# Kernel tuning notes

Measured on AMD Instinct MI355X. Metric: run time of the kernel, lower is better.

The kernel has to match this reference:

```python
import jax, jax.numpy as jnp
import numpy as np

# Module hyperparameters (from init_kwargs / config defaults)
LOCAL_WINDOW = 128
GLOBAL_BUDGET = 64
ATT_BUDGET = 0.05
RANDOM_BUDGET = 0.1

B, S, D = 4, 4096, 1024


def setup_inputs() -> dict:
    key = jax.random.key(0)
    k1, k2 = jax.random.split(key)
    return {
        "hidden_states": jax.random.normal(k1, (B, S, D), dtype=jnp.float32),
        "attention_mask": jnp.ones((B, S), dtype=jnp.int32),
        "W_imp": jax.random.normal(k2, (1, D), dtype=jnp.float32) * 0.02,
    }


def _build_sparse_mask(hidden_states, attention_mask, W_imp):
    b, s, d = hidden_states.shape
    valid = attention_mask.astype(bool)                       # [b, s]
    # base mask: valid x valid, with causal constraint (is_decoder=True)
    i = jnp.arange(s)[:, None]
    j = jnp.arange(s)[None, :]
    causal = j <= i                                            # [s, s]
    base = (valid[:, None, :] & valid[:, :, None]) & causal[None]

    # 1) local causal sliding window: query i attends keys in [i-W+1, i]
    diff = i - j
    local = (diff >= 0) & (diff < LOCAL_WINDOW)                # [s, s]
    sparse = jnp.broadcast_to(local[None], (b, s, s))
    selected = jnp.broadcast_to(local.any(axis=0)[None], (b, s))

    # 2) global tokens via importance projection + top-k
    base_budget = min(GLOBAL_BUDGET, max(1, int(s * ATT_BUDGET)))
    scores = jnp.einsum('bsd,d->bs', hidden_states, W_imp[0])  # [b, s]
    scores = jnp.where(valid, scores, -jnp.inf)
    _, top_idx = jax.lax.top_k(scores, base_budget)            # [b, k]
    global_tokens = jnp.zeros((b, s), bool).at[
        jnp.arange(b)[:, None], top_idx].set(True)             # [b, s]
    # globals attend to everything and are attended by everything
    sparse = sparse | global_tokens[:, None, :] | global_tokens[:, :, None]
    selected = selected | global_tokens

    # 3) structured random tokens: deterministic strided selection
    r_budget = min(s, max(1, int(s * RANDOM_BUDGET)))
    stride = max(1, s // r_budget)
    rand_idx = (jnp.arange(r_budget) * stride) % s
    random_1d = jnp.zeros((s,), bool).at[rand_idx].set(True)
    random_tokens = jnp.broadcast_to(random_1d[None], (b, s))  # [b, s]
    sparse = sparse | random_tokens[:, None, :] | random_tokens[:, :, None]
    selected = selected | random_tokens

    # re-apply validity + causality
    sparse = sparse & base
    return sparse, selected, global_tokens, random_tokens


def reference(hidden_states, attention_mask, W_imp):
    b, s, _ = hidden_states.shape
    sparse, selected, gtok, rtok = _build_sparse_mask(
        hidden_states, attention_mask, W_imp)
    total_connections = sparse.sum(axis=(1, 2))
    attention_efficiency = total_connections.astype(jnp.float32) / float(s * s)
    # return sparse mask as float (the form consumed by attention), plus stats
    return (sparse.astype(jnp.float32), selected, attention_efficiency)
```

## Files before the change

kernel.cpp:

```cpp
#include <hip/hip_runtime.h>
#include <math.h>

#define BATCH 4
#define SEQ   4096
#define DIM   1024
#define TOPK  64
#define RSTRIDE 10
#define RBUDGET 409
#define LOCALW  128

typedef float nfloat4 __attribute__((ext_vector_type(4)));

#define WS_SCORES_OFF 0
#define WS_FLAGS_OFF  (BATCH * SEQ * sizeof(float))

__global__ void scores_kernel(const float* __restrict__ hs,
                              const int* __restrict__ amask,
                              const float* __restrict__ W,
                              float* __restrict__ scores) {
    int row  = blockIdx.x * 4 + (threadIdx.x >> 6);
    int lane = threadIdx.x & 63;
    const float4* h4 = (const float4*)(hs + (size_t)row * DIM);
    const float4* w4 = (const float4*)W;
    float acc = 0.0f;
#pragma unroll
    for (int k = 0; k < DIM / 4 / 64; ++k) {
        float4 h = h4[lane + 64 * k];
        float4 w = w4[lane + 64 * k];
        acc += h.x * w.x + h.y * w.y + h.z * w.z + h.w * w.w;
    }
#pragma unroll
    for (int off = 32; off; off >>= 1) acc += __shfl_down(acc, off, 64);
    if (lane == 0)
        scores[row] = amask[row] ? acc : -INFINITY;
}

__global__ void topk_fused_kernel(const float* __restrict__ scores,
                                  const int* __restrict__ amask,
                                  unsigned char* __restrict__ flags,
                                  float* __restrict__ out_selected,
                                  float* __restrict__ out_eff) {
    __shared__ unsigned int su[SEQ];
    __shared__ int cumH[SEQ];
    __shared__ unsigned char gsel[SEQ];
    __shared__ unsigned char sflags[SEQ];
    __shared__ unsigned int hist[257];
    __shared__ unsigned int sufA[257];
    __shared__ unsigned int sufB[257];
    __shared__ unsigned int bcast[2];
    __shared__ int tvA[256], tvB[256], thA[256], thB[256], red[256];

    int b = blockIdx.x, t = threadIdx.x;

    for (int k = t; k < SEQ; k += 256) {
        float s = scores[b * SEQ + k];
        unsigned int x = __float_as_uint(s);
        su[k] = (x & 0x80000000u) ? ~x : (x | 0x80000000u);
        gsel[k] = 0;
    }
    __syncthreads();

    unsigned int prefixVal = 0;
    unsigned int remaining = TOPK;
#pragma unroll
    for (int pass = 0; pass < 4; ++pass) {
        int shift = 24 - 8 * pass;
        unsigned int highmask = (pass == 0) ? 0u : (0xFFFFFFFFu << (shift + 8));

        hist[t] = 0;
        if (t == 0) hist[256] = 0;
        __syncthreads();
#pragma unroll
        for (int e = 0; e < SEQ / 256; ++e) {
            unsigned int u = su[t * (SEQ / 256) + e];
            if ((u & highmask) == prefixVal)
                atomicAdd(&hist[(u >> shift) & 0xFFu], 1u);
        }
        __syncthreads();

        sufA[t] = hist[t];
        if (t == 0) sufA[256] = 0;
        __syncthreads();
        unsigned int* src = sufA;
        unsigned int* dst = sufB;
        for (int d = 1; d < 256; d <<= 1) {
            unsigned int v = src[t] + ((t + d < 256) ? src[t + d] : 0u);
            dst[t] = v;
            if (t == 0) dst[256] = 0;
            __syncthreads();
            unsigned int* tmp = src; src = dst; dst = tmp;
        }
        if (src[t] >= remaining && src[t + 1] < remaining) {
            bcast[0] = (unsigned int)t;
            bcast[1] = remaining - src[t + 1];
        }
        __syncthreads();
        prefixVal |= (bcast[0] << shift);
        remaining = bcast[1];
        __syncthreads();
    }

    unsigned int T = prefixVal;
    unsigned int myeq = 0;
#pragma unroll
    for (int e = 0; e < SEQ / 256; ++e)
        if (su[t * (SEQ / 256) + e] == T) myeq++;
    sufA[t] = myeq;
    __syncthreads();
    {
        unsigned int* src = sufA;
        unsigned int* dst = sufB;
        for (int d = 1; d < 256; d <<= 1) {
            unsigned int v = src[t] + ((t >= d) ? src[t - d] : 0u);
            dst[t] = v;
            __syncthreads();
            unsigned int* tmp = src; src = dst; dst = tmp;
        }
        unsigned int taken = src[t] - myeq;
#pragma unroll
        for (int e = 0; e < SEQ / 256; ++e) {
            int idx = t * (SEQ / 256) + e;
            unsigned int u = su[idx];
            if (u > T) gsel[idx] = 1;
            else if (u == T) { if (taken < remaining) gsel[idx] = 1; taken++; }
        }
    }
    __syncthreads();

    for (int k = t; k < SEQ; k += 256) {
        int valid = (amask[b * SEQ + k] != 0) ? 1 : 0;
        int g = gsel[k];
        int r = ((k % RSTRIDE) == 0 && (k / RSTRIDE) < RBUDGET) ? 1 : 0;
        unsigned char f = (unsigned char)(valid | (g << 1) | (r << 2));
        flags[b * SEQ + k] = f;
        sflags[k] = f;
        out_selected[b * SEQ + k] = 1.0f;
    }
    __syncthreads();

    int* cumV = (int*)su;
    int lv[16], lh[16];
    int sv = 0, sh = 0;
#pragma unroll
    for (int e = 0; e < 16; ++e) {
        unsigned char f = sflags[t * 16 + e];
        int v = f & 1;
        int h = v & (((f & 6) != 0) ? 1 : 0);
        sv += v; sh += h;
        lv[e] = sv; lh[e] = sh;
    }
    tvA[t] = sv; thA[t] = sh;
    __syncthreads();
    int* vsrc = tvA; int* vdst = tvB;
    int* hsrc = thA; int* hdst = thB;
    for (int d = 1; d < 256; d <<= 1) {
        int av = vsrc[t] + ((t >= d) ? vsrc[t - d] : 0);
        int ah = hsrc[t] + ((t >= d) ? hsrc[t - d] : 0);
        vdst[t] = av; hdst[t] = ah;
        __syncthreads();
        int* tmp = vsrc; vsrc = vdst; vdst = tmp;
        tmp = hsrc; hsrc = hdst; hdst = tmp;
    }
    int bv = vsrc[t] - sv, bh = hsrc[t] - sh;
#pragma unroll
    for (int e = 0; e < 16; ++e) {
        cumV[t * 16 + e] = lv[e] + bv;
        cumH[t * 16 + e] = lh[e] + bh;
    }
    __syncthreads();

    int cnt = 0;
#pragma unroll
    for (int e = 0; e < 16; ++e) {
        int i = t * 16 + e;
        unsigned char f = sflags[i];
        int validI = f & 1;
        int hotI = (f & 6) != 0;
        int c;
        if (hotI) c = cumV[i];
        else {
            int w = (i >= LOCALW) ? (cumV[i] - cumV[i - LOCALW]) : cumV[i];
            int g = (i >= LOCALW) ? cumH[i - LOCALW] : 0;
            c = w + g;
        }
        cnt += validI ? c : 0;
    }
    red[t] = cnt;
    __syncthreads();
    for (int s2 = 128; s2; s2 >>= 1) {
        if (t < s2) red[t] += red[t + s2];
        __syncthreads();
    }
    if (t == 0)
        out_eff[b] = (float)red[0] * (1.0f / ((float)SEQ * (float)SEQ));
}

#define MASK_BLOCKS 8192
__global__ void __launch_bounds__(256) mask_kernel(
        const unsigned char* __restrict__ flags,
        float* __restrict__ out) {
    const uchar4* f4all = (const uchar4*)flags;
    nfloat4* out4 = (nfloat4*)out;
    int p = blockIdx.x * 256 + threadIdx.x;
    const int stride = MASK_BLOCKS * 256;
#pragma unroll
    for (int it = 0; it < (BATCH * SEQ * SEQ / 4) / (MASK_BLOCKS * 256); ++it) {
        int row = p >> 10;
        int i = row & (SEQ - 1);
        int bbase = (row >> 12) << 10;
        unsigned char fi = flags[row];
        int validI = fi & 1;
        int hotI = (fi & 6) != 0;
        int jg = p & 1023;
        uchar4 fj = f4all[bbase + jg];
        unsigned char fja[4] = {fj.x, fj.y, fj.z, fj.w};
        int j0 = jg << 2;
        nfloat4 v;
#pragma unroll
        for (int e = 0; e < 4; ++e) {
            int j = j0 + e;
            unsigned char f = fja[e];
            int one = (j <= i) & validI & (int)(f & 1)
                    & (((i - j) < LOCALW) | hotI | (int)((f & 6) != 0));
            v[e] = one ? 1.0f : 0.0f;
        }
        out4[p] = v;
        p += stride;
    }
}

extern "C" void kernel_launch(void* const* d_in, const int* in_sizes, int n_in,
                              void* d_out, int out_size, void* d_ws, size_t ws_size,
                              hipStream_t stream) {
    const float* hs    = (const float*)d_in[0];
    const int*   amask = (const int*)d_in[1];
    const float* W     = (const float*)d_in[2];

    char* ws = (char*)d_ws;
    float*         scores = (float*)(ws + WS_SCORES_OFF);
    unsigned char* flags  = (unsigned char*)(ws + WS_FLAGS_OFF);

    float* out_sparse   = (float*)d_out;
    float* out_selected = out_sparse + (size_t)BATCH * SEQ * SEQ;
    float* out_eff      = out_selected + BATCH * SEQ;

    scores_kernel<<<BATCH * SEQ / 4, 256, 0, stream>>>(hs, amask, W, scores);
    topk_fused_kernel<<<BATCH, 256, 0, stream>>>(scores, amask, flags,
                                                 out_selected, out_eff);
    mask_kernel<<<MASK_BLOCKS, 256, 0, stream>>>(flags, out_sparse);
}
```

Before: 337.7 us.

## Fuse scores, top-k and mask into one persistent kernel with grid barriers

Merges the three kernels into a single persistent kernel of 1008 blocks that uses software grid barriers. While four blocks run the top-k and efficiency computation, the remaining blocks write the zero upper-triangle half of the mask, so that store traffic overlaps the serial top-k phase. After the barrier only the lower triangle is computed from the flags. This relies on every block being co-resident for the spin barrier and adds a small init kernel to reset the barrier counters.

```diff
diff --git a/kernel.cpp b/kernel.cpp
--- a/kernel.cpp
+++ b/kernel.cpp
@@ -9,223 +9,265 @@
 #define RBUDGET 409
 #define LOCALW  128
 
+#define NBLK  1008
+#define NTOPK 4
+
 typedef float nfloat4 __attribute__((ext_vector_type(4)));
 
 #define WS_SCORES_OFF 0
 #define WS_FLAGS_OFF  (BATCH * SEQ * sizeof(float))
-
-__global__ void scores_kernel(const float* __restrict__ hs,
-                              const int* __restrict__ amask,
-                              const float* __restrict__ W,
-                              float* __restrict__ scores) {
-    int row  = blockIdx.x * 4 + (threadIdx.x >> 6);
-    int lane = threadIdx.x & 63;
-    const float4* h4 = (const float4*)(hs + (size_t)row * DIM);
-    const float4* w4 = (const float4*)W;
-    float acc = 0.0f;
-#pragma unroll
-    for (int k = 0; k < DIM / 4 / 64; ++k) {
-        float4 h = h4[lane + 64 * k];
-        float4 w = w4[lane + 64 * k];
-        acc += h.x * w.x + h.y * w.y + h.z * w.z + h.w * w.w;
-    }
-#pragma unroll
-    for (int off = 32; off; off >>= 1) acc += __shfl_down(acc, off, 64);
-    if (lane == 0)
-        scores[row] = amask[row] ? acc : -INFINITY;
-}
-
-__global__ void topk_fused_kernel(const float* __restrict__ scores,
-                                  const int* __restrict__ amask,
-                                  unsigned char* __restrict__ flags,
-                                  float* __restrict__ out_selected,
-                                  float* __restrict__ out_eff) {
+#define WS_SYNC_OFF   (WS_FLAGS_OFF + BATCH * SEQ)
+
+__global__ void init_sync_kernel(unsigned int* sync) {
+    if (threadIdx.x < 4) sync[threadIdx.x] = 0u;
+}
+
+__device__ __forceinline__ void grid_barrier(unsigned int* cnt,
+                                             unsigned int* flag) {
+    __syncthreads();
+    if (threadIdx.x == 0) {
+        __threadfence();
+        unsigned int old = atomicAdd(cnt, 1u);
+        if (old == (unsigned int)NBLK - 1u) {
+            __hip_atomic_store(flag, 1u, __ATOMIC_RELEASE,
+                               __HIP_MEMORY_SCOPE_AGENT);
+        } else {
+            while (__hip_atomic_load(flag, __ATOMIC_ACQUIRE,
+                                     __HIP_MEMORY_SCOPE_AGENT) == 0u) {}
+        }
+        __threadfence();
+    }
+    __syncthreads();
+}
+
+__global__ void __launch_bounds__(256, 4) fused_kernel(
+        const float* __restrict__ hs,
+        const int* __restrict__ amask,
+        const float* __restrict__ W,
+        float* scores,
+        unsigned char* flags,
+        unsigned int* sync,
+        float* out_sparse,
+        float* __restrict__ out_selected,
+        float* __restrict__ out_eff) {
     __shared__ unsigned int su[SEQ];
-    __shared__ int cumH[SEQ];
-    __shared__ unsigned char gsel[SEQ];
+    __shared__ unsigned short cumH[SEQ];
     __shared__ unsigned char sflags[SEQ];
     __shared__ unsigned int hist[257];
     __shared__ unsigned int sufA[257];
     __shared__ unsigned int sufB[257];
     __shared__ unsigned int bcast[2];
-    __shared__ int tvA[256], tvB[256], thA[256], thB[256], red[256];
-
-    int b = blockIdx.x, t = threadIdx.x;
-
-    for (int k = t; k < SEQ; k += 256) {
-        float s = scores[b * SEQ + k];
-        unsigned int x = __float_as_uint(s);
-        su[k] = (x & 0x80000000u) ? ~x : (x | 0x80000000u);
-        gsel[k] = 0;
-    }
-    __syncthreads();
-
-    unsigned int prefixVal = 0;
-    unsigned int remaining = TOPK;
-#pragma unroll
-    for (int pass = 0; pass < 4; ++pass) {
-        int shift = 24 - 8 * pass;
-        unsigned int highmask = (pass == 0) ? 0u : (0xFFFFFFFFu << (shift + 8));
-
-        hist[t] = 0;
-        if (t == 0) hist[256] = 0;
-        __syncthreads();
-#pragma unroll
-        for (int e = 0; e < SEQ / 256; ++e) {
-            unsigned int u = su[t * (SEQ / 256) + e];
-            if ((u & highmask) == prefixVal)
-                atomicAdd(&hist[(u >> shift) & 0xFFu], 1u);
-        }
-        __syncthreads();
-
-        sufA[t] = hist[t];
-        if (t == 0) sufA[256] = 0;
-        __syncthreads();
-        unsigned int* src = sufA;
-        unsigned int* dst = sufB;
+    __shared__ int tvA[256], tvB[256], thA[256], thB[256];
+    __shared__ int red[256];
+
+    const int bid = blockIdx.x;
+    const int t = threadIdx.x;
+
+    {
+        int lane = t & 63;
+        int wid = t >> 6;
+        const float4* w4 = (const float4*)W;
+        for (int row = bid * 4 + wid; row < BATCH * SEQ; row += NBLK * 4) {
+            const float4* h4 = (const float4*)(hs + (size_t)row * DIM);
+            float acc = 0.0f;
+#pragma unroll
+            for (int k = 0; k < DIM / 4 / 64; ++k) {
+                float4 h = h4[lane + 64 * k];
+                float4 w = w4[lane + 64 * k];
+                acc += h.x * w.x + h.y * w.y + h.z * w.z + h.w * w.w;
+            }
+#pragma unroll
+            for (int off = 32; off; off >>= 1) acc += __shfl_down(acc, off, 64);
+            if (lane == 0)
+                scores[row] = amask[row] ? acc : -INFINITY;
+        }
+        int gid = bid * 256 + t;
+        if (gid < BATCH * SEQ) out_selected[gid] = 1.0f;
+    }
+    grid_barrier(&sync[0], &sync[1]);
+
+    if (bid < NTOPK) {
+        int b = bid;
+        for (int k = t; k < SEQ; k += 256) {
+            float s = scores[b * SEQ + k];
+            unsigned int x = __float_as_uint(s);
+            su[k] = (x & 0x80000000u) ? ~x : (x | 0x80000000u);
+            sflags[k] = 0;
+        }
+        __syncthreads();
+
+        unsigned int prefixVal = 0;
+        unsigned int remaining = TOPK;
+#pragma unroll
+        for (int pass = 0; pass < 4; ++pass) {
+            int shift = 24 - 8 * pass;
+            unsigned int highmask = (pass == 0) ? 0u : (0xFFFFFFFFu << (shift + 8));
+
+            hist[t] = 0;
+            if (t == 0) hist[256] = 0;
+            __syncthreads();
+#pragma unroll
+            for (int e = 0; e < SEQ / 256; ++e) {
+                unsigned int u = su[t * (SEQ / 256) + e];
+                if ((u & highmask) == prefixVal)
+                    atomicAdd(&hist[(u >> shift) & 0xFFu], 1u);
+            }
+            __syncthreads();
+
+            sufA[t] = hist[t];
+            if (t == 0) sufA[256] = 0;
+            __syncthreads();
+            unsigned int* src = sufA;
+            unsigned int* dst = sufB;
+            for (int d = 1; d < 256; d <<= 1) {
+                unsigned int v = src[t] + ((t + d < 256) ? src[t + d] : 0u);
+                dst[t] = v;
+                if (t == 0) dst[256] = 0;
+                __syncthreads();
+                unsigned int* tmp = src; src = dst; dst = tmp;
+            }
+            if (src[t] >= remaining && src[t + 1] < remaining) {
+                bcast[0] = (unsigned int)t;
+                bcast[1] = remaining - src[t + 1];
+            }
+            __syncthreads();
+            prefixVal |= (bcast[0] << shift);
+            remaining = bcast[1];
+            __syncthreads();
+        }
+
+        unsigned int T = prefixVal;
+        unsigned int myeq = 0;
+#pragma unroll
+        for (int e = 0; e < SEQ / 256; ++e)
+            if (su[t * (SEQ / 256) + e] == T) myeq++;
+        sufA[t] = myeq;
+        __syncthreads();
+        {
+            unsigned int* src = sufA;
+            unsigned int* dst = sufB;
+            for (int d = 1; d < 256; d <<= 1) {
+                unsigned int v = src[t] + ((t >= d) ? src[t - d] : 0u);
+                dst[t] = v;
+                __syncthreads();
+                unsigned int* tmp = src; src = dst; dst = tmp;
+            }
+            unsigned int taken = src[t] - myeq;
+#pragma unroll
+            for (int e = 0; e < SEQ / 256; ++e) {
+                int idx = t * (SEQ / 256) + e;
+                unsigned int u = su[idx];
+                if (u > T) sflags[idx] |= 2;
+                else if (u == T) { if (taken < remaining) sflags[idx] |= 2; taken++; }
+            }
+        }
+        __syncthreads();
+
+        for (int k = t; k < SEQ; k += 256) {
+            int valid = (amask[b * SEQ + k] != 0) ? 1 : 0;
+            int g = (sflags[k] >> 1) & 1;
+            int r = ((k % RSTRIDE) == 0 && (k / RSTRIDE) < RBUDGET) ? 1 : 0;
+            unsigned char f = (unsigned char)(valid | (g << 1) | (r << 2));
+            sflags[k] = f;
+            flags[b * SEQ + k] = f;
+        }
+        __syncthreads();
+
+        int* cumV = (int*)su;
+        int lv[16], lh[16];
+        int sv = 0, sh = 0;
+#pragma unroll
+        for (int e = 0; e < 16; ++e) {
+            unsigned char f = sflags[t * 16 + e];
+            int v = f & 1;
+            int h = v & (((f & 6) != 0) ? 1 : 0);
+            sv += v; sh += h;
+            lv[e] = sv; lh[e] = sh;
+        }
+        tvA[t] = sv; thA[t] = sh;
+        __syncthreads();
+        int* vsrc = tvA; int* vdst = tvB;
+        int* hsrc = thA; int* hdst = thB;
         for (int d = 1; d < 256; d <<= 1) {
-            unsigned int v = src[t] + ((t + d < 256) ? src[t + d] : 0u);
-            dst[t] = v;
-            if (t == 0) dst[256] = 0;
-            __syncthreads();
-            unsigned int* tmp = src; src = dst; dst = tmp;
-        }
-        if (src[t] >= remaining && src[t + 1] < remaining) {
-            bcast[0] = (unsigned int)t;
-            bcast[1] = remaining - src[t + 1];
-        }
-        __syncthreads();
-        prefixVal |= (bcast[0] << shift);
-        remaining = bcast[1];
-        __syncthreads();
-    }
-
-    unsigned int T = prefixVal;
-    unsigned int myeq = 0;
-#pragma unroll
-    for (int e = 0; e < SEQ / 256; ++e)
-        if (su[t * (SEQ / 256) + e] == T) myeq++;
-    sufA[t] = myeq;
-    __syncthreads();
+            int av = vsrc[t] + ((t >= d) ? vsrc[t - d] : 0);
+            int ah = hsrc[t] + ((t >= d) ? hsrc[t - d] : 0);
+            vdst[t] = av; hdst[t] = ah;
+            __syncthreads();
+            int* tmp = vsrc; vsrc = vdst; vdst = tmp;
+            tmp = hsrc; hsrc = hdst; hdst = tmp;
+        }
+        int bv = vsrc[t] - sv, bh = hsrc[t] - sh;
+#pragma unroll
+        for (int e = 0; e < 16; ++e) {
+            cumV[t * 16 + e] = lv[e] + bv;
+            cumH[t * 16 + e] = (unsigned short)(lh[e] + bh);
+        }
+        __syncthreads();
+
+        int cnt = 0;
+#pragma unroll
+        for (int e = 0; e < 16; ++e) {
+            int i = t * 16 + e;
+            unsigned char f = sflags[i];
+            int validI = f & 1;
+            int hotI = (f & 6) != 0;
+            int c;
+            if (hotI) c = cumV[i];
+            else {
+                int w = (i >= LOCALW) ? (cumV[i] - cumV[i - LOCALW]) : cumV[i];
+                int g = (i >= LOCALW) ? (int)cumH[i - LOCALW] : 0;
+                c = w + g;
+            }
+            cnt += validI ? c : 0;
+        }
+        red[t] = cnt;
+        __syncthreads();
+        for (int s2 = 128; s2; s2 >>= 1) {
+            if (t < s2) red[t] += red[t + s2];
+            __syncthreads();
+        }
+        if (t == 0)
+            out_eff[b] = (float)red[0] * (1.0f / ((float)SEQ * (float)SEQ));
+    } else {
+        const nfloat4 zero4 = {0.0f, 0.0f, 0.0f, 0.0f};
+        nfloat4* out4 = (nfloat4*)out_sparse;
+        for (int row = bid - NTOPK; row < BATCH * SEQ; row += NBLK - NTOPK) {
+            int i = row & (SEQ - 1);
+            int g0 = (i >> 2) + 1;
+            nfloat4* o = out4 + (size_t)row * (SEQ / 4);
+            for (int g = g0 + t; g < SEQ / 4; g += 256)
+                o[g] = zero4;
+        }
+    }
+    grid_barrier(&sync[2], &sync[3]);
+
     {
-        unsigned int* src = sufA;
-        unsigned int* dst = sufB;
-        for (int d = 1; d < 256; d <<= 1) {
-            unsigned int v = src[t] + ((t >= d) ? src[t - d] : 0u);
-            dst[t] = v;
-            __syncthreads();
-            unsigned int* tmp = src; src = dst; dst = tmp;
-        }
-        unsigned int taken = src[t] - myeq;
-#pragma unroll
-        for (int e = 0; e < SEQ / 256; ++e) {
-            int idx = t * (SEQ / 256) + e;
-            unsigned int u = su[idx];
-            if (u > T) gsel[idx] = 1;
-            else if (u == T) { if (taken < remaining) gsel[idx] = 1; taken++; }
-        }
-    }
-    __syncthreads();
-
-    for (int k = t; k < SEQ; k += 256) {
-        int valid = (amask[b * SEQ + k] != 0) ? 1 : 0;
-        int g = gsel[k];
-        int r = ((k % RSTRIDE) == 0 && (k / RSTRIDE) < RBUDGET) ? 1 : 0;
-        unsigned char f = (unsigned char)(valid | (g << 1) | (r << 2));
-        flags[b * SEQ + k] = f;
-        sflags[k] = f;
-        out_selected[b * SEQ + k] = 1.0f;
-    }
-    __syncthreads();
-
-    int* cumV = (int*)su;
-    int lv[16], lh[16];
-    int sv = 0, sh = 0;
-#pragma unroll
-    for (int e = 0; e < 16; ++e) {
-        unsigned char f = sflags[t * 16 + e];
-        int v = f & 1;
-        int h = v & (((f & 6) != 0) ? 1 : 0);
-        sv += v; sh += h;
-        lv[e] = sv; lh[e] = sh;
-    }
-    tvA[t] = sv; thA[t] = sh;
-    __syncthreads();
-    int* vsrc = tvA; int* vdst = tvB;
-    int* hsrc = thA; int* hdst = thB;
-    for (int d = 1; d < 256; d <<= 1) {
-        int av = vsrc[t] + ((t >= d) ? vsrc[t - d] : 0);
-        int ah = hsrc[t] + ((t >= d) ? hsrc[t - d] : 0);
-        vdst[t] = av; hdst[t] = ah;
-        __syncthreads();
-        int* tmp = vsrc; vsrc = vdst; vdst = tmp;
-        tmp = hsrc; hsrc = hdst; hdst = tmp;
-    }
-    int bv = vsrc[t] - sv, bh = hsrc[t] - sh;
-#pragma unroll
-    for (int e = 0; e < 16; ++e) {
-        cumV[t * 16 + e] = lv[e] + bv;
-        cumH[t * 16 + e] = lh[e] + bh;
-    }
-    __syncthreads();
-
-    int cnt = 0;
-#pragma unroll
-    for (int e = 0; e < 16; ++e) {
-        int i = t * 16 + e;
-        unsigned char f = sflags[i];
-        int validI = f & 1;
-        int hotI = (f & 6) != 0;
-        int c;
-        if (hotI) c = cumV[i];
-        else {
-            int w = (i >= LOCALW) ? (cumV[i] - cumV[i - LOCALW]) : cumV[i];
-            int g = (i >= LOCALW) ? cumH[i - LOCALW] : 0;
-            c = w + g;
-        }
-        cnt += validI ? c : 0;
-    }
-    red[t] = cnt;
-    __syncthreads();
-    for (int s2 = 128; s2; s2 >>= 1) {
-        if (t < s2) red[t] += red[t + s2];
-        __syncthreads();
-    }
-    if (t == 0)
-        out_eff[b] = (float)red[0] * (1.0f / ((float)SEQ * (float)SEQ));
-}
-
-#define MASK_BLOCKS 8192
-__global__ void __launch_bounds__(256) mask_kernel(
-        const unsigned char* __restrict__ flags,
-        float* __restrict__ out) {
-    const uchar4* f4all = (const uchar4*)flags;
-    nfloat4* out4 = (nfloat4*)out;
-    int p = blockIdx.x * 256 + threadIdx.x;
-    const int stride = MASK_BLOCKS * 256;
-#pragma unroll
-    for (int it = 0; it < (BATCH * SEQ * SEQ / 4) / (MASK_BLOCKS * 256); ++it) {
-        int row = p >> 10;
-        int i = row & (SEQ - 1);
-        int bbase = (row >> 12) << 10;
-        unsigned char fi = flags[row];
-        int validI = fi & 1;
-        int hotI = (fi & 6) != 0;
-        int jg = p & 1023;
-        uchar4 fj = f4all[bbase + jg];
-        unsigned char fja[4] = {fj.x, fj.y, fj.z, fj.w};
-        int j0 = jg << 2;
-        nfloat4 v;
-#pragma unroll
-        for (int e = 0; e < 4; ++e) {
-            int j = j0 + e;
-            unsigned char f = fja[e];
-            int one = (j <= i) & validI & (int)(f & 1)
-                    & (((i - j) < LOCALW) | hotI | (int)((f & 6) != 0));
-            v[e] = one ? 1.0f : 0.0f;
-        }
-        out4[p] = v;
-        p += stride;
+        const uchar4* f4all = (const uchar4*)flags;
+        nfloat4* out4 = (nfloat4*)out_sparse;
+        for (int row = bid; row < BATCH * SEQ; row += NBLK) {
+            int i = row & (SEQ - 1);
+            int bbase = (row >> 12) << 10;
+            unsigned char fi = flags[row];
+            int validI = fi & 1;
+            int hotI = (fi & 6) != 0;
+            int gmax = i >> 2;
+            nfloat4* o = out4 + (size_t)row * (SEQ / 4);
+            for (int g = t; g <= gmax; g += 256) {
+                uchar4 fj = f4all[bbase + g];
+                unsigned char fja[4] = {fj.x, fj.y, fj.z, fj.w};
+                int j0 = g << 2;
+                nfloat4 v;
+#pragma unroll
+                for (int e = 0; e < 4; ++e) {
+                    int j = j0 + e;
+                    unsigned char f = fja[e];
+                    int one = (j <= i) & validI & (int)(f & 1)
+                            & (((i - j) < LOCALW) | hotI | (int)((f & 6) != 0));
+                    v[e] = one ? 1.0f : 0.0f;
+                }
+                o[g] = v;
+            }
+        }
     }
 }
 
@@ -239,13 +281,13 @@
     char* ws = (char*)d_ws;
     float*         scores = (float*)(ws + WS_SCORES_OFF);
     unsigned char* flags  = (unsigned char*)(ws + WS_FLAGS_OFF);
+    unsigned int*  sync   = (unsigned int*)(ws + WS_SYNC_OFF);
 
     float* out_sparse   = (float*)d_out;
     float* out_selected = out_sparse + (size_t)BATCH * SEQ * SEQ;
     float* out_eff      = out_selected + BATCH * SEQ;
 
-    scores_kernel<<<BATCH * SEQ / 4, 256, 0, stream>>>(hs, amask, W, scores);
-    topk_fused_kernel<<<BATCH, 256, 0, stream>>>(scores, amask, flags,
-                                                 out_selected, out_eff);
-    mask_kernel<<<MASK_BLOCKS, 256, 0, stream>>>(flags, out_sparse);
-}
+    init_sync_kernel<<<1, 64, 0, stream>>>(sync);
+    fused_kernel<<<NBLK, 256, 0, stream>>>(hs, amask, W, scores, flags, sync,
+                                           out_sparse, out_selected, out_eff);
+}
```

Measured after the change: 637.7 us. 88.8% more time.
